# Kernel tuning notes

Hardware: AMD Instinct MI355X
Metric: run time of the kernel (lower is better)

The kernel has to match this reference:

```python
import jax, jax.numpy as jnp
import numpy as np
from jax import lax

V, E, H, T = 50000, 256, 512, 16  # vocab, embed_dim, hidden_dim, num_tags
B, S = 32, 512
C = 128          # conv channels
HD = H // 2      # per-direction LSTM hidden


def setup_inputs() -> dict:
    key = jax.random.key(0)
    ks = jax.random.split(key, 20)
    g = lambda k, shape, s=0.05: jax.random.normal(k, shape, jnp.float32) * s
    return {
        "x": jax.random.randint(ks[0], (B, S), 0, V),
        "mask": jnp.ones((B, S), jnp.int32),
        "tags": jax.random.randint(ks[1], (B, S), 0, T),
        "embed_table": g(ks[2], (V, E), 0.1),
        "conv_w": g(ks[3], (C, E, 3)),
        "conv_b": g(ks[4], (C,)),
        "wih_f": g(ks[5], (4 * HD, C)),
        "whh_f": g(ks[6], (4 * HD, HD)),
        "bih_f": g(ks[7], (4 * HD,)),
        "bhh_f": g(ks[8], (4 * HD,)),
        "wih_b": g(ks[9], (4 * HD, C)),
        "whh_b": g(ks[10], (4 * HD, HD)),
        "bih_b": g(ks[11], (4 * HD,)),
        "bhh_b": g(ks[12], (4 * HD,)),
        "fc_w": g(ks[13], (T, H)),
        "fc_b": g(ks[14], (T,)),
        "start_trans": g(ks[15], (T,), 0.1),
        "end_trans": g(ks[16], (T,), 0.1),
        "trans": g(ks[17], (T, T), 0.1),
    }


def _lstm_dir(xs, wih, whh, bih, bhh, reverse):
    # xs: [S, B, D] -> hidden states [S, B, HD], PyTorch gate order i,f,g,o
    b = xs.shape[1]
    h0 = jnp.zeros((b, whh.shape[1]), xs.dtype)

    def step(carry, xt):
        h, c = carry
        gates = xt @ wih.T + h @ whh.T + bih + bhh  # [B, 4*HD]
        i, f, g, o = jnp.split(gates, 4, axis=-1)
        c = jax.nn.sigmoid(f) * c + jax.nn.sigmoid(i) * jnp.tanh(g)
        h = jax.nn.sigmoid(o) * jnp.tanh(c)
        return (h, c), h

    _, hs = lax.scan(step, (h0, h0), xs, reverse=reverse)
    return hs


def _crf_nll(emissions, tg, m, start_trans, end_trans, trans):
    # emissions [S,B,T], tg [S,B] int, m [S,B] float -> per-seq -loglik mean
    bidx = jnp.arange(emissions.shape[1])
    # numerator: score of the gold path
    score = start_trans[tg[0]] + emissions[0, bidx, tg[0]]

    def num_step(s, inp):
        prev_t, cur_t, em, mi = inp
        return s + (trans[prev_t, cur_t] + em[bidx, cur_t]) * mi, None

    score, _ = lax.scan(num_step, score, (tg[:-1], tg[1:], emissions[1:], m[1:]))
    seq_ends = m.sum(0).astype(jnp.int32) - 1
    score = score + end_trans[tg[seq_ends, bidx]]
    # denominator: forward algorithm (log partition)
    alpha = start_trans + emissions[0]  # [B,T]

    def den_step(a, inp):
        em, mi = inp
        nxt = jax.nn.logsumexp(a[:, :, None] + trans[None] + em[:, None, :], axis=1)
        return jnp.where(mi[:, None] > 0, nxt, a), None

    alpha, _ = lax.scan(den_step, alpha, (emissions[1:], m[1:]))
    logz = jax.nn.logsumexp(alpha + end_trans[None], axis=1)
    return -jnp.mean(score - logz)


def reference(x, mask, tags, embed_table, conv_w, conv_b, wih_f, whh_f, bih_f,
              bhh_f, wih_b, whh_b, bih_b, bhh_b, fc_w, fc_b, start_trans,
              end_trans, trans):
    emb = embed_table[x]                       # [B,S,E]
    xc = jnp.transpose(emb, (0, 2, 1))         # [B,E,S]
    conv = lax.conv_general_dilated(xc, conv_w, (1,), [(1, 1)],
                                    dimension_numbers=("NCH", "OIH", "NCH"))
    feat = jax.nn.relu(conv + conv_b[None, :, None])   # [B,C,S]
    xs = jnp.transpose(feat, (2, 0, 1))        # [S,B,C]
    hf = _lstm_dir(xs, wih_f, whh_f, bih_f, bhh_f, False)
    hb = _lstm_dir(xs, wih_b, whh_b, bih_b, bhh_b, True)
    h = jnp.concatenate([hf, hb], axis=-1)     # [S,B,H]
    emissions = h @ fc_w.T + fc_b              # [S,B,T]
    m = jnp.transpose(mask, (1, 0)).astype(emissions.dtype)
    tg = jnp.transpose(tags, (1, 0))
    return _crf_nll(emissions, tg, m, start_trans, end_trans, trans)
```

## Files before the change

kernel.cpp:

```cpp
#include <hip/hip_runtime.h>
#include <hip/hip_bf16.h>

constexpr int NB = 32, NS = 512, NE = 256, NC = 128, NHD = 256, NG = 1024, NT = 16, NH = 512;

typedef float f32x4 __attribute__((ext_vector_type(4)));

__device__ __forceinline__ unsigned short f2bf(float f) {
    unsigned u = __float_as_uint(f);
    u += 0x7fffu + ((u >> 16) & 1u);
    return (unsigned short)(u >> 16);
}
__device__ __forceinline__ float bf2f(unsigned short s) {
    return __uint_as_float(((unsigned)s) << 16);
}
__device__ __forceinline__ float vexp2(float x) {
    float r; asm("v_exp_f32 %0, %1" : "=v"(r) : "v"(x)); return r;
}
__device__ __forceinline__ float vrcp(float x) {
    float r; asm("v_rcp_f32 %0, %1" : "=v"(r) : "v"(x)); return r;
}
__device__ __forceinline__ float vlog2(float x) {
    float r; asm("v_log_f32 %0, %1" : "=v"(r) : "v"(x)); return r;
}
__device__ __forceinline__ unsigned char f2fp8(float v) {
    int r = __builtin_amdgcn_cvt_pk_fp8_f32(v, 0.f, 0, false);
    return (unsigned char)(r & 0xff);
}
__device__ __constant__ float KSC[4] = {-1.442695041f, -1.442695041f, 2.885390082f, -1.442695041f};

__global__ void k_prep_convw(const float* __restrict__ w, float* __restrict__ wT) {
    int i = blockIdx.x * 256 + threadIdx.x;
    if (i >= 768 * 128) return;
    int e3 = i >> 7, c = i & 127;
    wT[i] = w[c * 768 + e3];
}

__global__ void k_prep_scale(const float* __restrict__ whh_f, const float* __restrict__ whh_b,
                             float* __restrict__ scale) {
    int d = blockIdx.y;
    const float* src = d ? whh_b : whh_f;
    int col = blockIdx.x * 256 + threadIdx.x;
    if (col >= 1024) return;
    int j = col >> 2, g = col & 3;
    const float* p = src + (size_t)(g * 256 + j) * 256;
    float m = 0.f;
    for (int k = 0; k < 256; ++k) m = fmaxf(m, fabsf(p[k]));
    scale[d * 1024 + col] = (m > 0.f) ? (m * (1.f / 448.f)) : 1.f;
}

__global__ void k_prep_whh_frag8(const float* __restrict__ whh_f, const float* __restrict__ whh_b,
                                 const float* __restrict__ scale, unsigned char* __restrict__ whhF8) {
    int i = blockIdx.x * 256 + threadIdx.x;
    if (i >= (1 << 19)) return;
    int e = i & 7;
    int lane = (i >> 3) & 63;
    int g = (i >> 9) & 3;
    int kt = (i >> 11) & 7;
    int w = (i >> 14) & 15;
    int d = (i >> 18) & 1;
    const float* src = d ? whh_b : whh_f;
    int j = w * 16 + (lane & 15);
    int k = kt * 32 + (lane >> 4) * 8 + e;
    float sc = scale[d * 1024 + j * 4 + g];
    float v = src[(g * 256 + j) * 256 + k] / sc;
    whhF8[i] = f2fp8(v);
}

__global__ void k_prep_wih(const float* __restrict__ wih_f, const float* __restrict__ wih_b,
                           float* __restrict__ wihT) {
    int d = blockIdx.y;
    const float* src = d ? wih_b : wih_f;
    int i = blockIdx.x * 256 + threadIdx.x;
    if (i >= NC * NG) return;
    int g = i & 3, j = (i >> 2) & 255, e = i >> 10;
    wihT[(size_t)d * NC * NG + i] = src[(g * 256 + j) * 128 + e];
}

__global__ void k_prep_bias(const float* __restrict__ bih_f, const float* __restrict__ bhh_f,
                            const float* __restrict__ bih_b, const float* __restrict__ bhh_b,
                            float* __restrict__ bias2) {
    int d = blockIdx.y;
    const float* bi = d ? bih_b : bih_f;
    const float* bh = d ? bhh_b : bhh_f;
    int i = blockIdx.x * 256 + threadIdx.x;
    if (i >= NG) return;
    int g = i & 3, j = i >> 2;
    bias2[(size_t)d * NG + i] = bi[g * 256 + j] + bh[g * 256 + j];
}

__global__ __launch_bounds__(128) void k_conv(const int* __restrict__ x,
                                              const float* __restrict__ table,
                                              const float* __restrict__ wT,
                                              const float* __restrict__ conv_b,
                                              float* __restrict__ feat) {
    int b = blockIdx.y;
    int s0 = blockIdx.x * 8;
    int c = threadIdx.x;
    __shared__ float win[10][NE];
    for (int i = 0; i < 10; ++i) {
        int s = s0 - 1 + i;
        if (s < 0 || s >= NS) {
            for (int e = c; e < NE; e += 128) win[i][e] = 0.f;
        } else {
            int tok = x[b * NS + s];
            const float* row = table + (size_t)tok * NE;
            for (int e = c; e < NE; e += 128) win[i][e] = row[e];
        }
    }
    __syncthreads();
    float acc[8];
    float bc = conv_b[c];
#pragma unroll
    for (int p = 0; p < 8; ++p) acc[p] = bc;
    for (int e = 0; e < NE; ++e) {
        float r[10];
#pragma unroll
        for (int i = 0; i < 10; ++i) r[i] = win[i][e];
#pragma unroll
        for (int k = 0; k < 3; ++k) {
            float wv = wT[(e * 3 + k) * NC + c];
#pragma unroll
            for (int p = 0; p < 8; ++p) acc[p] += wv * r[p + k];
        }
    }
#pragma unroll
    for (int p = 0; p < 8; ++p) {
        feat[((size_t)b * NS + s0 + p) * NC + c] = fmaxf(acc[p], 0.f);
    }
}

__global__ __launch_bounds__(256) void k_xgate(const float* __restrict__ feat,
                                               const float* __restrict__ wihT,
                                               const float* __restrict__ bias2,
                                               unsigned short* __restrict__ xg) {
    int d = blockIdx.y;
    int p0 = blockIdx.x * 16;
    int j = threadIdx.x;
    __shared__ float fv[16][NC];
    for (int i = threadIdx.x; i < 16 * NC; i += 256) {
        int p = i >> 7, e = i & 127;
        int idx = p0 + p;
        int s = idx >> 5, b = idx & 31;
        fv[p][e] = feat[((size_t)b * NS + s) * NC + e];
    }
    __syncthreads();
    const float* W = wihT + (size_t)d * NC * NG;
    float b0 = bias2[(size_t)d * NG + j * 4 + 0];
    float b1 = bias2[(size_t)d * NG + j * 4 + 1];
    float b2 = bias2[(size_t)d * NG + j * 4 + 2];
    float b3 = bias2[(size_t)d * NG + j * 4 + 3];
    float acc[16][4];
#pragma unroll
    for (int p = 0; p < 16; ++p) {
        acc[p][0] = b0; acc[p][1] = b1; acc[p][2] = b2; acc[p][3] = b3;
    }
    for (int e = 0; e < NC; ++e) {
        float4 w4 = *(const float4*)(W + ((size_t)e * 256 + j) * 4);
#pragma unroll
        for (int p = 0; p < 16; ++p) {
            float fe = fv[p][e];
            acc[p][0] += fe * w4.x;
            acc[p][1] += fe * w4.y;
            acc[p][2] += fe * w4.z;
            acc[p][3] += fe * w4.w;
        }
    }
#pragma unroll
    for (int p = 0; p < 16; ++p) {
        ushort4 o;
        o.x = f2bf(acc[p][0] * KSC[0]); o.y = f2bf(acc[p][1] * KSC[1]);
        o.z = f2bf(acc[p][2] * KSC[2]); o.w = f2bf(acc[p][3] * KSC[3]);
        unsigned short* dst = xg + (size_t)d * NS * NB * NG + ((size_t)(p0 + p) * 256 + j) * 4;
        *(ushort4*)dst = o;
    }
}

__global__ __launch_bounds__(1024, 1) void k_lstm2(const unsigned char* __restrict__ whhF8,
                                                   const float* __restrict__ scale,
                                                   const unsigned short* __restrict__ xg,
                                                   float* __restrict__ hcat) {
    int bid = blockIdx.x;
    int d = bid >> 1, bh = bid & 1;
    int tid = threadIdx.x;
    int w = tid >> 6, l = tid & 63;
    int l15 = l & 15, lq = l >> 4;
    __shared__ unsigned char hbuf[2][16][280];
    for (int i = tid; i < 2 * 16 * 280; i += 1024) (&hbuf[0][0][0])[i] = 0;
    unsigned long long wf[32];
    const unsigned char* wp = whhF8 + ((size_t)(d * 16 + w) << 14) + (size_t)l * 8;
#pragma unroll
    for (int f = 0; f < 32; ++f) wf[f] = *(const unsigned long long*)(wp + f * 512);
    int cell = w * 16 + l15;
    float csc[4];
#pragma unroll
    for (int g = 0; g < 4; ++g)
        csc[g] = scale[d * 1024 + cell * 4 + g] * KSC[g];
    const unsigned short* XG = xg + (size_t)d * NS * NB * NG;
    float cst[4] = {};
    __syncthreads();
    int cur = 0;
    unsigned long long xq[4];
    {
        int s0 = d ? (NS - 1) : 0;
#pragma unroll
        for (int r = 0; r < 4; ++r)
            xq[r] = *(const unsigned long long*)(
                XG + (size_t)(s0 * 32 + bh * 16 + lq * 4 + r) * 1024 + cell * 4);
    }
    for (int step = 0; step < NS; ++step) {
        int s = d ? (NS - 1 - step) : step;
        unsigned long long xn[4];
        {
            int stn = (step + 1 < NS) ? step + 1 : step;
            int sn = d ? (NS - 1 - stn) : stn;
#pragma unroll
            for (int r = 0; r < 4; ++r)
                xn[r] = *(const unsigned long long*)(
                    XG + (size_t)(sn * 32 + bh * 16 + lq * 4 + r) * 1024 + cell * 4);
        }
        f32x4 acc[4];
#pragma unroll
        for (int g = 0; g < 4; ++g) acc[g] = (f32x4){0.f, 0.f, 0.f, 0.f};
#pragma unroll
        for (int kt = 0; kt < 8; ++kt) {
            unsigned long long a = *(const unsigned long long*)&hbuf[cur][l15][kt * 32 + lq * 8];
#pragma unroll
            for (int g = 0; g < 4; ++g)
                acc[g] = __builtin_amdgcn_mfma_f32_16x16x32_fp8_fp8(
                    (long long)a, (long long)wf[kt * 4 + g], acc[g], 0, 0, 0);
        }
        int nxt = cur ^ 1;
#pragma unroll
        for (int r = 0; r < 4; ++r) {
            unsigned long long xv = xq[r];
            float pi = fmaf(acc[0][r], csc[0], bf2f((unsigned short)xv));
            float pf = fmaf(acc[1][r], csc[1], bf2f((unsigned short)(xv >> 16)));
            float pg = fmaf(acc[2][r], csc[2], bf2f((unsigned short)(xv >> 32)));
            float po = fmaf(acc[3][r], csc[3], bf2f((unsigned short)(xv >> 48)));
            float si = vrcp(1.f + vexp2(pi));
            float sf = vrcp(1.f + vexp2(pf));
            float tg = fmaf(-2.f, vrcp(1.f + vexp2(pg)), 1.f);
            float so = vrcp(1.f + vexp2(po));
            float c = fmaf(sf, cst[r], si * tg);
            cst[r] = c;
            float tc = fmaf(-2.f, vrcp(1.f + vexp2(2.885390082f * c)), 1.f);
            float h = so * tc;
            int b = lq * 4 + r;
            __builtin_nontemporal_store(h,
                hcat + (size_t)(s * 32 + bh * 16 + b) * NH + d * NHD + cell);
            hbuf[nxt][b][cell] = f2fp8(h);
        }
        __syncthreads();
        cur = nxt;
#pragma unroll
        for (int r = 0; r < 4; ++r) xq[r] = xn[r];
    }
}

__global__ __launch_bounds__(256) void k_fc(const float* __restrict__ hcat,
                                            const float* __restrict__ fc_w,
                                            const float* __restrict__ fc_b,
                                            float* __restrict__ em) {
    int p0 = blockIdx.x * 16;
    __shared__ float hv[16][NH];
    for (int i = threadIdx.x; i < 16 * NH; i += 256) {
        int p = i >> 9, hh = i & 511;
        hv[p][hh] = hcat[(size_t)(p0 + p) * NH + hh];
    }
    __syncthreads();
    int p = threadIdx.x >> 4, t = threadIdx.x & 15;
    const float* fw = fc_w + t * NH;
    float acc = fc_b[t];
#pragma unroll 8
    for (int hh = 0; hh < NH; ++hh) acc += hv[p][hh] * fw[hh];
    em[(size_t)(p0 + p) * NT + t] = acc;
}

__global__ __launch_bounds__(64) void k_crf(const float* __restrict__ em,
                                            const int* __restrict__ tags,
                                            const int* __restrict__ mask,
                                            const float* __restrict__ start_t,
                                            const float* __restrict__ end_t,
                                            const float* __restrict__ trans,
                                            float* __restrict__ res) {
    int b = blockIdx.x;
    int tid = threadIdx.x;
    __shared__ float em_sh[NS * NT];
    __shared__ float tr[NT * NT];
    __shared__ float alpha_sh[NT];
    __shared__ float msk[NS];
    __shared__ float sc_sh;
    for (int i = tid; i < NT * NT; i += 64) tr[i] = trans[i];
    for (int i = tid; i < NS * NT; i += 64) {
        int s = i >> 4, t = i & 15;
        em_sh[i] = em[((size_t)s * NB + b) * NT + t];
    }
    for (int s = tid; s < NS; s += 64) msk[s] = (float)mask[b * NS + s];
    __syncthreads();
    float part = 0.f, msum = 0.f;
    for (int s = tid; s < NS; s += 64) msum += msk[s];
    for (int s = 1 + tid; s < NS; s += 64) {
        int pv = tags[b * NS + s - 1], cu = tags[b * NS + s];
        part += (tr[pv * NT + cu] + em_sh[s * NT + cu]) * msk[s];
    }
#pragma unroll
    for (int o = 32; o > 0; o >>= 1) {
        part += __shfl_down(part, o);
        msum += __shfl_down(msum, o);
    }
    if (tid == 0) {
        int t0 = tags[b * NS];
        int send = (int)msum - 1;
        sc_sh = start_t[t0] + em_sh[t0] + part + end_t[tags[b * NS + send]];
    }
    if (tid < NT) alpha_sh[tid] = start_t[tid] + em_sh[tid];
    __syncthreads();
    int t_to = tid >> 2, q = tid & 3;
    for (int s = 1; s < NS; ++s) {
        float v0 = alpha_sh[q * 4 + 0] + tr[(q * 4 + 0) * NT + t_to];
        float v1 = alpha_sh[q * 4 + 1] + tr[(q * 4 + 1) * NT + t_to];
        float v2 = alpha_sh[q * 4 + 2] + tr[(q * 4 + 2) * NT + t_to];
        float v3 = alpha_sh[q * 4 + 3] + tr[(q * 4 + 3) * NT + t_to];
        float mx = fmaxf(fmaxf(v0, v1), fmaxf(v2, v3));
        mx = fmaxf(mx, __shfl_xor(mx, 1));
        mx = fmaxf(mx, __shfl_xor(mx, 2));
        float nmx = -1.442695041f * mx;
        float ss = vexp2(fmaf(v0, 1.442695041f, nmx)) + vexp2(fmaf(v1, 1.442695041f, nmx))
                 + vexp2(fmaf(v2, 1.442695041f, nmx)) + vexp2(fmaf(v3, 1.442695041f, nmx));
        ss += __shfl_xor(ss, 1);
        ss += __shfl_xor(ss, 2);
        float nv = mx + 0.6931471806f * vlog2(ss) + em_sh[s * NT + t_to];
        float old = alpha_sh[t_to];
        nv = (msk[s] > 0.f) ? nv : old;
        __syncthreads();
        if (q == 0) alpha_sh[t_to] = nv;
        __syncthreads();
    }
    if (tid == 0) {
        float mx = -1e30f;
        for (int t = 0; t < NT; ++t) mx = fmaxf(mx, alpha_sh[t] + end_t[t]);
        float sum = 0.f;
        for (int t = 0; t < NT; ++t) sum += vexp2(1.442695041f * (alpha_sh[t] + end_t[t] - mx));
        res[b] = sc_sh - (mx + 0.6931471806f * vlog2(sum));
    }
}

__global__ void k_final(const float* __restrict__ res, float* __restrict__ out) {
    int tid = threadIdx.x;
    float v = (tid < NB) ? res[tid] : 0.f;
#pragma unroll
    for (int o = 32; o > 0; o >>= 1) v += __shfl_down(v, o);
    if (tid == 0) out[0] = -v / NB;
}

constexpr size_t SZ_FEAT  = (size_t)NB * NS * NC * 4;
constexpr size_t SZ_WT    = (size_t)768 * 128 * 4;
constexpr size_t SZ_WHHF8 = (size_t)(1 << 19);
constexpr size_t SZ_SCALE = (size_t)2 * 1024 * 4;
constexpr size_t SZ_WIHT  = (size_t)2 * NC * NG * 4;
constexpr size_t SZ_BIAS  = (size_t)2 * NG * 4;
constexpr size_t SZ_XG    = (size_t)2 * NS * NB * NG * 2;
constexpr size_t SZ_HCAT  = (size_t)NS * NB * NH * 4;
constexpr size_t SZ_EM    = (size_t)NS * NB * NT * 4;

constexpr size_t OFF_FEAT  = 0;
constexpr size_t OFF_WT    = OFF_FEAT + SZ_FEAT;
constexpr size_t OFF_WHHF8 = OFF_WT + SZ_WT;
constexpr size_t OFF_SCALE = OFF_WHHF8 + SZ_WHHF8;
constexpr size_t OFF_WIHT  = OFF_SCALE + SZ_SCALE;
constexpr size_t OFF_BIAS  = OFF_WIHT + SZ_WIHT;
constexpr size_t OFF_XG    = OFF_BIAS + SZ_BIAS;
constexpr size_t OFF_HCAT  = OFF_XG + SZ_XG;
constexpr size_t OFF_EM    = OFF_HCAT + SZ_HCAT;
constexpr size_t OFF_RES   = OFF_EM + SZ_EM;

extern "C" void kernel_launch(void* const* d_in, const int* in_sizes, int n_in,
                              void* d_out, int out_size, void* d_ws, size_t ws_size,
                              hipStream_t stream) {
    const int* x        = (const int*)d_in[0];
    const int* mask     = (const int*)d_in[1];
    const int* tags     = (const int*)d_in[2];
    const float* table  = (const float*)d_in[3];
    const float* conv_w = (const float*)d_in[4];
    const float* conv_b = (const float*)d_in[5];
    const float* wih_f  = (const float*)d_in[6];
    const float* whh_f  = (const float*)d_in[7];
    const float* bih_f  = (const float*)d_in[8];
    const float* bhh_f  = (const float*)d_in[9];
    const float* wih_b  = (const float*)d_in[10];
    const float* whh_b  = (const float*)d_in[11];
    const float* bih_b  = (const float*)d_in[12];
    const float* bhh_b  = (const float*)d_in[13];
    const float* fc_w   = (const float*)d_in[14];
    const float* fc_b   = (const float*)d_in[15];
    const float* start_t = (const float*)d_in[16];
    const float* end_t  = (const float*)d_in[17];
    const float* trans  = (const float*)d_in[18];

    char* ws = (char*)d_ws;
    float* feat = (float*)(ws + OFF_FEAT);
    float* wT   = (float*)(ws + OFF_WT);
    unsigned char* whhF8 = (unsigned char*)(ws + OFF_WHHF8);
    float* scale = (float*)(ws + OFF_SCALE);
    float* wihT = (float*)(ws + OFF_WIHT);
    float* bias2 = (float*)(ws + OFF_BIAS);
    unsigned short* xg = (unsigned short*)(ws + OFF_XG);
    float* hcat = (float*)(ws + OFF_HCAT);
    float* em   = (float*)(ws + OFF_EM);
    float* res  = (float*)(ws + OFF_RES);

    k_prep_convw<<<dim3(384), 256, 0, stream>>>(conv_w, wT);
    k_prep_scale<<<dim3(4, 2), 256, 0, stream>>>(whh_f, whh_b, scale);
    k_prep_whh_frag8<<<dim3(2048), 256, 0, stream>>>(whh_f, whh_b, scale, whhF8);
    k_prep_wih<<<dim3(512, 2), 256, 0, stream>>>(wih_f, wih_b, wihT);
    k_prep_bias<<<dim3(4, 2), 256, 0, stream>>>(bih_f, bhh_f, bih_b, bhh_b, bias2);
    k_conv<<<dim3(NS / 8, NB), 128, 0, stream>>>(x, table, wT, conv_b, feat);
    k_xgate<<<dim3(NS * NB / 16, 2), 256, 0, stream>>>(feat, wihT, bias2, xg);
    k_lstm2<<<dim3(4), 1024, 0, stream>>>(whhF8, scale, xg, hcat);
    k_fc<<<dim3(NS * NB / 16), 256, 0, stream>>>(hcat, fc_w, fc_b, em);
    k_crf<<<dim3(NB), 64, 0, stream>>>(em, tags, mask, start_t, end_t, trans, res);
    k_final<<<dim3(1), 64, 0, stream>>>(res, (float*)d_out);
}
```

Before: 1.381 ms.

## Compute LSTM input gates with bf16 MFMA and store intermediates in bf16

Rewrites the input-gate projection as a bf16 MFMA (16x16x32) kernel. The weights are pre-swizzled into fragment layout, with the gate scale folded into the weights and bias. The conv features and the LSTM hidden outputs are stored as bf16 instead of fp32, which halves their memory traffic. This adds bf16 rounding to the features and hidden states. The total time is likely dominated by the sequential LSTM kernel, so the gain is limited to the xgate kernel and memory traffic.

```diff
diff --git a/kernel.cpp b/kernel.cpp
--- a/kernel.cpp
+++ b/kernel.cpp
@@ -4,6 +4,7 @@
 constexpr int NB = 32, NS = 512, NE = 256, NC = 128, NHD = 256, NG = 1024, NT = 16, NH = 512;
 
 typedef float f32x4 __attribute__((ext_vector_type(4)));
+typedef short bf16x8 __attribute__((ext_vector_type(8)));
 
 __device__ __forceinline__ unsigned short f2bf(float f) {
     unsigned u = __float_as_uint(f);
@@ -66,33 +67,39 @@
     whhF8[i] = f2fp8(v);
 }
 
-__global__ void k_prep_wih(const float* __restrict__ wih_f, const float* __restrict__ wih_b,
-                           float* __restrict__ wihT) {
-    int d = blockIdx.y;
+__global__ void k_prep_wih_frag(const float* __restrict__ wih_f, const float* __restrict__ wih_b,
+                                unsigned short* __restrict__ wihF) {
+    int i = blockIdx.x * 256 + threadIdx.x;
+    if (i >= (1 << 18)) return;
+    int e = i & 7;
+    int lane = (i >> 3) & 63;
+    int kt = (i >> 9) & 3;
+    int ctg = (i >> 11) & 63;
+    int d = (i >> 17) & 1;
     const float* src = d ? wih_b : wih_f;
-    int i = blockIdx.x * 256 + threadIdx.x;
-    if (i >= NC * NG) return;
-    int g = i & 3, j = (i >> 2) & 255, e = i >> 10;
-    wihT[(size_t)d * NC * NG + i] = src[(g * 256 + j) * 128 + e];
+    int row = lane & 15;
+    int cell = ctg * 4 + (row >> 2), g = row & 3;
+    int k = kt * 32 + (lane >> 4) * 8 + e;
+    wihF[i] = f2bf(src[(g * 256 + cell) * 128 + k] * KSC[g]);
 }
 
 __global__ void k_prep_bias(const float* __restrict__ bih_f, const float* __restrict__ bhh_f,
                             const float* __restrict__ bih_b, const float* __restrict__ bhh_b,
-                            float* __restrict__ bias2) {
+                            float* __restrict__ bias2s) {
     int d = blockIdx.y;
     const float* bi = d ? bih_b : bih_f;
     const float* bh = d ? bhh_b : bhh_f;
     int i = blockIdx.x * 256 + threadIdx.x;
     if (i >= NG) return;
     int g = i & 3, j = i >> 2;
-    bias2[(size_t)d * NG + i] = bi[g * 256 + j] + bh[g * 256 + j];
+    bias2s[(size_t)d * NG + i] = (bi[g * 256 + j] + bh[g * 256 + j]) * KSC[g];
 }
 
 __global__ __launch_bounds__(128) void k_conv(const int* __restrict__ x,
                                               const float* __restrict__ table,
                                               const float* __restrict__ wT,
                                               const float* __restrict__ conv_b,
-                                              float* __restrict__ feat) {
+                                              unsigned short* __restrict__ feat) {
     int b = blockIdx.y;
     int s0 = blockIdx.x * 8;
     int c = threadIdx.x;
@@ -125,60 +132,49 @@
     }
 #pragma unroll
     for (int p = 0; p < 8; ++p) {
-        feat[((size_t)b * NS + s0 + p) * NC + c] = fmaxf(acc[p], 0.f);
-    }
-}
-
-__global__ __launch_bounds__(256) void k_xgate(const float* __restrict__ feat,
-                                               const float* __restrict__ wihT,
-                                               const float* __restrict__ bias2,
+        feat[((size_t)b * NS + s0 + p) * NC + c] = f2bf(fmaxf(acc[p], 0.f));
+    }
+}
+
+__global__ __launch_bounds__(256) void k_xgate(const unsigned short* __restrict__ feat,
+                                               const unsigned short* __restrict__ wihF,
+                                               const float* __restrict__ bias2s,
                                                unsigned short* __restrict__ xg) {
     int d = blockIdx.y;
     int p0 = blockIdx.x * 16;
-    int j = threadIdx.x;
-    __shared__ float fv[16][NC];
-    for (int i = threadIdx.x; i < 16 * NC; i += 256) {
-        int p = i >> 7, e = i & 127;
-        int idx = p0 + p;
-        int s = idx >> 5, b = idx & 31;
-        fv[p][e] = feat[((size_t)b * NS + s) * NC + e];
-    }
-    __syncthreads();
-    const float* W = wihT + (size_t)d * NC * NG;
-    float b0 = bias2[(size_t)d * NG + j * 4 + 0];
-    float b1 = bias2[(size_t)d * NG + j * 4 + 1];
-    float b2 = bias2[(size_t)d * NG + j * 4 + 2];
-    float b3 = bias2[(size_t)d * NG + j * 4 + 3];
-    float acc[16][4];
-#pragma unroll
-    for (int p = 0; p < 16; ++p) {
-        acc[p][0] = b0; acc[p][1] = b1; acc[p][2] = b2; acc[p][3] = b3;
-    }
-    for (int e = 0; e < NC; ++e) {
-        float4 w4 = *(const float4*)(W + ((size_t)e * 256 + j) * 4);
-#pragma unroll
-        for (int p = 0; p < 16; ++p) {
-            float fe = fv[p][e];
-            acc[p][0] += fe * w4.x;
-            acc[p][1] += fe * w4.y;
-            acc[p][2] += fe * w4.z;
-            acc[p][3] += fe * w4.w;
-        }
-    }
-#pragma unroll
-    for (int p = 0; p < 16; ++p) {
-        ushort4 o;
-        o.x = f2bf(acc[p][0] * KSC[0]); o.y = f2bf(acc[p][1] * KSC[1]);
-        o.z = f2bf(acc[p][2] * KSC[2]); o.w = f2bf(acc[p][3] * KSC[3]);
-        unsigned short* dst = xg + (size_t)d * NS * NB * NG + ((size_t)(p0 + p) * 256 + j) * 4;
-        *(ushort4*)dst = o;
+    int tid = threadIdx.x;
+    int w = tid >> 6, l = tid & 63;
+    int l15 = l & 15, lq = l >> 4;
+    int p = p0 + l15, b = p & 31, s = p >> 5;
+    const unsigned short* fp = feat + ((size_t)b * NS + s) * NC + lq * 8;
+    bf16x8 bf[4];
+#pragma unroll
+    for (int kt = 0; kt < 4; ++kt) bf[kt] = *(const bf16x8*)(fp + kt * 32);
+    const unsigned short* WF = wihF + ((size_t)d << 17);
+    unsigned short* XGD = xg + (size_t)d * NS * NB * NG;
+#pragma unroll
+    for (int ct = 0; ct < 16; ++ct) {
+        int ctg = w * 16 + ct;
+        int cell = ctg * 4 + lq;
+        float4 bv = *(const float4*)(bias2s + (size_t)d * NG + cell * 4);
+        f32x4 acc = {bv.x, bv.y, bv.z, bv.w};
+#pragma unroll
+        for (int kt = 0; kt < 4; ++kt) {
+            bf16x8 af = *(const bf16x8*)(WF + (((size_t)ctg * 4 + kt) * 64 + l) * 8);
+            acc = __builtin_amdgcn_mfma_f32_16x16x32_bf16(af, bf[kt], acc, 0, 0, 0);
+        }
+        unsigned long long hp = (unsigned long long)f2bf(acc[0])
+                              | ((unsigned long long)f2bf(acc[1]) << 16)
+                              | ((unsigned long long)f2bf(acc[2]) << 32)
+                              | ((unsigned long long)f2bf(acc[3]) << 48);
+        *(unsigned long long*)(XGD + (size_t)p * 1024 + cell * 4) = hp;
     }
 }
 
 __global__ __launch_bounds__(1024, 1) void k_lstm2(const unsigned char* __restrict__ whhF8,
                                                    const float* __restrict__ scale,
                                                    const unsigned short* __restrict__ xg,
-                                                   float* __restrict__ hcat) {
+                                                   unsigned short* __restrict__ hcat) {
     int bid = blockIdx.x;
     int d = bid >> 1, bh = bid & 1;
     int tid = threadIdx.x;
@@ -246,7 +242,7 @@
             float tc = fmaf(-2.f, vrcp(1.f + vexp2(2.885390082f * c)), 1.f);
             float h = so * tc;
             int b = lq * 4 + r;
-            __builtin_nontemporal_store(h,
+            __builtin_nontemporal_store(f2bf(h),
                 hcat + (size_t)(s * 32 + bh * 16 + b) * NH + d * NHD + cell);
             hbuf[nxt][b][cell] = f2fp8(h);
         }
@@ -257,7 +253,7 @@
     }
 }
 
-__global__ __launch_bounds__(256) void k_fc(const float* __restrict__ hcat,
+__global__ __launch_bounds__(256) void k_fc(const unsigned short* __restrict__ hcat,
                                             const float* __restrict__ fc_w,
                                             const float* __restrict__ fc_b,
                                             float* __restrict__ em) {
@@ -265,7 +261,7 @@
     __shared__ float hv[16][NH];
     for (int i = threadIdx.x; i < 16 * NH; i += 256) {
         int p = i >> 9, hh = i & 511;
-        hv[p][hh] = hcat[(size_t)(p0 + p) * NH + hh];
+        hv[p][hh] = bf2f(hcat[(size_t)(p0 + p) * NH + hh]);
     }
     __syncthreads();
     int p = threadIdx.x >> 4, t = threadIdx.x & 15;
@@ -353,22 +349,22 @@
     if (tid == 0) out[0] = -v / NB;
 }
 
-constexpr size_t SZ_FEAT  = (size_t)NB * NS * NC * 4;
+constexpr size_t SZ_FEAT  = (size_t)NB * NS * NC * 2;
 constexpr size_t SZ_WT    = (size_t)768 * 128 * 4;
 constexpr size_t SZ_WHHF8 = (size_t)(1 << 19);
 constexpr size_t SZ_SCALE = (size_t)2 * 1024 * 4;
-constexpr size_t SZ_WIHT  = (size_t)2 * NC * NG * 4;
+constexpr size_t SZ_WIHF  = (size_t)(1 << 18) * 2;
 constexpr size_t SZ_BIAS  = (size_t)2 * NG * 4;
 constexpr size_t SZ_XG    = (size_t)2 * NS * NB * NG * 2;
-constexpr size_t SZ_HCAT  = (size_t)NS * NB * NH * 4;
+constexpr size_t SZ_HCAT  = (size_t)NS * NB * NH * 2;
 constexpr size_t SZ_EM    = (size_t)NS * NB * NT * 4;
 
 constexpr size_t OFF_FEAT  = 0;
 constexpr size_t OFF_WT    = OFF_FEAT + SZ_FEAT;
 constexpr size_t OFF_WHHF8 = OFF_WT + SZ_WT;
 constexpr size_t OFF_SCALE = OFF_WHHF8 + SZ_WHHF8;
-constexpr size_t OFF_WIHT  = OFF_SCALE + SZ_SCALE;
-constexpr size_t OFF_BIAS  = OFF_WIHT + SZ_WIHT;
+constexpr size_t OFF_WIHF  = OFF_SCALE + SZ_SCALE;
+constexpr size_t OFF_BIAS  = OFF_WIHF + SZ_WIHF;
 constexpr size_t OFF_XG    = OFF_BIAS + SZ_BIAS;
 constexpr size_t OFF_HCAT  = OFF_XG + SZ_XG;
 constexpr size_t OFF_EM    = OFF_HCAT + SZ_HCAT;
@@ -398,24 +394,24 @@
     const float* trans  = (const float*)d_in[18];
 
     char* ws = (char*)d_ws;
-    float* feat = (float*)(ws + OFF_FEAT);
+    unsigned short* feat = (unsigned short*)(ws + OFF_FEAT);
     float* wT   = (float*)(ws + OFF_WT);
     unsigned char* whhF8 = (unsigned char*)(ws + OFF_WHHF8);
     float* scale = (float*)(ws + OFF_SCALE);
-    float* wihT = (float*)(ws + OFF_WIHT);
-    float* bias2 = (float*)(ws + OFF_BIAS);
+    unsigned short* wihF = (unsigned short*)(ws + OFF_WIHF);
+    float* bias2s = (float*)(ws + OFF_BIAS);
     unsigned short* xg = (unsigned short*)(ws + OFF_XG);
-    float* hcat = (float*)(ws + OFF_HCAT);
+    unsigned short* hcat = (unsigned short*)(ws + OFF_HCAT);
     float* em   = (float*)(ws + OFF_EM);
     float* res  = (float*)(ws + OFF_RES);
 
     k_prep_convw<<<dim3(384), 256, 0, stream>>>(conv_w, wT);
     k_prep_scale<<<dim3(4, 2), 256, 0, stream>>>(whh_f, whh_b, scale);
     k_prep_whh_frag8<<<dim3(2048), 256, 0, stream>>>(whh_f, whh_b, scale, whhF8);
-    k_prep_wih<<<dim3(512, 2), 256, 0, stream>>>(wih_f, wih_b, wihT);
-    k_prep_bias<<<dim3(4, 2), 256, 0, stream>>>(bih_f, bhh_f, bih_b, bhh_b, bias2);
+    k_prep_wih_frag<<<dim3(1024), 256, 0, stream>>>(wih_f, wih_b, wihF);
+    k_prep_bias<<<dim3(4, 2), 256, 0, stream>>>(bih_f, bhh_f, bih_b, bhh_b, bias2s);
     k_conv<<<dim3(NS / 8, NB), 128, 0, stream>>>(x, table, wT, conv_b, feat);
-    k_xgate<<<dim3(NS * NB / 16, 2), 256, 0, stream>>>(feat, wihT, bias2, xg);
+    k_xgate<<<dim3(NS * NB / 16, 2), 256, 0, stream>>>(feat, wihF, bias2s, xg);
     k_lstm2<<<dim3(4), 1024, 0, stream>>>(whhF8, scale, xg, hcat);
     k_fc<<<dim3(NS * NB / 16), 256, 0, stream>>>(hcat, fc_w, fc_b, em);
     k_crf<<<dim3(NB), 64, 0, stream>>>(em, tags, mask, start_t, end_t, trans, res);
```

Result: faster. 1.351 ms (-2.2%).
